# Optimization experiments

Measured on AMD Instinct MI355X. Metric: run time of the kernel, lower is better.

## Reference

```python
import jax, jax.numpy as jnp
import numpy as np


def conv1d(x, w, b, pad):
    # x: [B,C,T], w: [O,I,K]
    y = jax.lax.conv_general_dilated(x, w, (1,), [(pad, pad)],
                                     dimension_numbers=('NCH', 'OIH', 'NCH'))
    return y + b[None, :, None]


def setup_inputs() -> dict:
    key = jax.random.key(0)
    ks = jax.random.split(key, 16)
    s = 0.05
    return {
        'x':    jax.random.normal(ks[0], (1024, 512), dtype=jnp.float32),
        'w1':   jax.random.normal(ks[1], (5, 1, 3), dtype=jnp.float32) * s,
        'b1':   jnp.zeros((5,), jnp.float32),
        'w2':   jax.random.normal(ks[2], (10, 5, 5), dtype=jnp.float32) * s,
        'b2':   jnp.zeros((10,), jnp.float32),
        'w3':   jax.random.normal(ks[3], (10, 10, 7), dtype=jnp.float32) * s,
        'b3':   jnp.zeros((10,), jnp.float32),
        'code': jax.random.uniform(ks[4], (10, 32), dtype=jnp.float32),
        'd1w':  jax.random.normal(ks[5], (10, 10, 5), dtype=jnp.float32) * s,
        'd1b':  jnp.zeros((10,), jnp.float32),
        'd2w':  jax.random.normal(ks[6], (10, 10, 5), dtype=jnp.float32) * s,
        'd2b':  jnp.zeros((10,), jnp.float32),
        'fcw':  jax.random.normal(ks[7], (512, 5120), dtype=jnp.float32) * 0.01,
        'fcb':  jnp.zeros((512,), jnp.float32),
    }


def reference(x, w1, b1, w2, b2, w3, b3, code, d1w, d1b, d2w, d2b, fcw, fcb):
    B = x.shape[0]
    h = x[:, None, :]                                   # [B,1,512]
    h = jax.nn.relu(conv1d(h, w1, b1, 1))               # [B,5,512]
    h = jax.nn.relu(conv1d(h, w2, b2, 2))               # [B,10,512]
    h = jnp.tanh(conv1d(h, w3, b3, 3))                  # [B,10,512]
    # squared distance: sum_c (h[b,c,t] - code[c,k])^2 -> [B,512,32]
    x2 = jnp.sum(h * h, axis=1)                         # [B,512]
    cross = jnp.einsum('bct,ck->btk', h, code)          # [B,512,32]
    c2 = jnp.sum(code * code, axis=0)                   # [32]
    dist = x2[:, :, None] - 2.0 * cross + c2[None, None, :]
    prob = jax.nn.softmax(-dist, axis=-1)               # [B,512,32]
    q = jnp.einsum('btk,ck->btc', prob, code)           # [B,512,10]
    h = q.transpose(0, 2, 1)                            # [B,10,512]
    h = jax.nn.relu(conv1d(h, d1w, d1b, 2))
    h = jax.nn.relu(conv1d(h, d2w, d2b, 2))
    flat = h.reshape(B, -1)                             # [B,5120]
    return jnp.tanh(flat @ fcw.T + fcb)                 # [B,512]
```

## Files before the change

kernel.cpp:

```cpp
#include <hip/hip_runtime.h>
#include <hip/hip_bf16.h>

#define TT 512
#define RS 16
#define RH 8
#define NROW 528
#define K_FC 5120

typedef _Float16 h8 __attribute__((ext_vector_type(8)));
typedef float f32x16 __attribute__((ext_vector_type(16)));
typedef __attribute__((address_space(1))) const void GAS;
typedef __attribute__((address_space(3))) void LAS;

__device__ __forceinline__ float fast_tanh(float v) {
    float e = __expf(2.0f * v);
    return 1.0f - 2.0f / (e + 1.0f);
}
__device__ __forceinline__ unsigned pk(float a, float b) {
    return __builtin_bit_cast(unsigned, __builtin_amdgcn_cvt_pkrtz(a, b));
}

__global__ __launch_bounds__(256) void prep_wtab_kernel(
    const float* __restrict__ w2, const float* __restrict__ w3,
    const float* __restrict__ d1w, const float* __restrict__ d2w,
    const float* __restrict__ code, uint4* __restrict__ wtab,
    unsigned* __restrict__ c2tab)
{
    const int i = blockIdx.x * 256 + threadIdx.x;
    if (i < 1600) {
        const int lane = i & 63;
        const int o = lane & 31;
        const int hi = lane >> 5;
        h8 v = {};
        if (i < 320) {
            const int j = i >> 6;
            #pragma unroll
            for (int e = 0; e < 8; ++e) {
                int k = hi * 8 + e;
                if (o < 10 && k < 5) v[e] = (_Float16)w2[(o * 5 + k) * 5 + j];
            }
        } else if (i < 768) {
            const int j = (i - 320) >> 6;
            #pragma unroll
            for (int e = 0; e < 8; ++e) {
                int k = hi * 8 + e;
                if (o < 10 && k < 10) v[e] = (_Float16)w3[(o * 10 + k) * 7 + j];
            }
        } else if (i < 1088) {
            const int j = (i - 768) >> 6;
            #pragma unroll
            for (int e = 0; e < 8; ++e) {
                int k = hi * 8 + e;
                if (o < 10 && k < 10) v[e] = (_Float16)d1w[(o * 10 + k) * 5 + j];
            }
        } else if (i < 1408) {
            const int j = (i - 1088) >> 6;
            #pragma unroll
            for (int e = 0; e < 8; ++e) {
                int k = hi * 8 + e;
                if (o < 10 && k < 10) v[e] = (_Float16)d2w[(o * 10 + k) * 5 + j];
            }
        } else if (i < 1472) {
            #pragma unroll
            for (int e = 0; e < 8; ++e) {
                int ch = hi * 8 + e;
                if (ch < 10) v[e] = (_Float16)(2.0f * code[ch * 32 + o]);
            }
        } else {
            const int ks = (i - 1472) >> 6;
            #pragma unroll
            for (int e = 0; e < 8; ++e) {
                int kc = ks * 16 + hi * 8 + e;
                if (o < 10) v[e] = (_Float16)code[o * 32 + kc];
            }
        }
        wtab[i] = __builtin_bit_cast(uint4, v);
    } else if (i < 1632) {
        int k = i - 1600;
        float s = 0.f;
        for (int c = 0; c < 10; ++c) { float cv = code[c * 32 + k]; s = fmaf(cv, cv, s); }
        c2tab[k] = __float_as_uint(4.0f - s);
    }
}

template<int J, int P, int ACT>
__device__ __forceinline__ void conv_stage(
    const _Float16* __restrict__ src, _Float16* __restrict__ dst,
    const uint4* __restrict__ wtab, int wbase, const float* __restrict__ bsrc)
{
    const int tid = threadIdx.x;
    const int lane = tid & 63;
    const int wv = tid >> 6;
    const int l31 = lane & 31;
    const int hi = lane >> 5;

    uint4 wf[J];
    #pragma unroll
    for (int j = 0; j < J; ++j) wf[j] = wtab[wbase + j * 64 + lane];
    float bias[6];
    #pragma unroll
    for (int r = 0; r < 6; ++r) {
        int m = (r & 3) + 8 * (r >> 2) + 4 * hi;
        bias[r] = (m < 10) ? bsrc[m] : 0.f;
    }

    #pragma unroll 2
    for (int tile = 0; tile < 4; ++tile) {
        const int tcol = wv * 128 + tile * 32 + l31;
        f32x16 acc = {};
        #pragma unroll
        for (int j = 0; j < J; ++j) {
            h8 bf = *(const h8*)(src + (tcol + RH - P + j) * RS + hi * 8);
            acc = __builtin_amdgcn_mfma_f32_32x32x16_f16(
                __builtin_bit_cast(h8, wf[j]), bf, acc, 0, 0, 0);
        }
        float v[6];
        #pragma unroll
        for (int r = 0; r < 6; ++r) {
            float t = acc[r] + bias[r];
            v[r] = (ACT == 0) ? fmaxf(t, 0.f) : fast_tanh(t);
        }
        unsigned* drow = (unsigned*)(dst + (tcol + RH) * RS);
        uint2 s1v; s1v.x = pk(v[0], v[1]); s1v.y = pk(v[2], v[3]);
        *(uint2*)(drow + hi * 2) = s1v;
        if (!hi) drow[4] = pk(v[4], v[5]);
    }
}

template<int J, int P>
__device__ __forceinline__ void conv_stage_flat(
    const _Float16* __restrict__ src, _Float16* __restrict__ flatrow,
    const uint4* __restrict__ wtab, int wbase, const float* __restrict__ bsrc)
{
    const int tid = threadIdx.x;
    const int lane = tid & 63;
    const int wv = tid >> 6;
    const int l31 = lane & 31;
    const int hi = lane >> 5;

    uint4 wf[J];
    #pragma unroll
    for (int j = 0; j < J; ++j) wf[j] = wtab[wbase + j * 64 + lane];
    float bias[6];
    #pragma unroll
    for (int r = 0; r < 6; ++r) {
        int m = (r & 3) + 8 * (r >> 2) + 4 * hi;
        bias[r] = (m < 10) ? bsrc[m] : 0.f;
    }

    #pragma unroll 2
    for (int tile = 0; tile < 4; ++tile) {
        const int tcol = wv * 128 + tile * 32 + l31;
        f32x16 acc = {};
        #pragma unroll
        for (int j = 0; j < J; ++j) {
            h8 bf = *(const h8*)(src + (tcol + RH - P + j) * RS + hi * 8);
            acc = __builtin_amdgcn_mfma_f32_32x32x16_f16(
                __builtin_bit_cast(h8, wf[j]), bf, acc, 0, 0, 0);
        }
        #pragma unroll
        for (int r = 0; r < 4; ++r)
            flatrow[(r + 4 * hi) * TT + tcol] = (_Float16)fmaxf(acc[r] + bias[r], 0.f);
        if (!hi) {
            flatrow[8 * TT + tcol] = (_Float16)fmaxf(acc[4] + bias[4], 0.f);
            flatrow[9 * TT + tcol] = (_Float16)fmaxf(acc[5] + bias[5], 0.f);
        }
    }
}

__device__ __forceinline__ void vq_stage(
    const _Float16* __restrict__ src, _Float16* __restrict__ dst,
    const uint4* __restrict__ wtab, const unsigned* __restrict__ c2tab)
{
    const int tid = threadIdx.x;
    const int lane = tid & 63;
    const int wv = tid >> 6;
    const int l31 = lane & 31;
    const int hi = lane >> 5;

    const h8 wcr = __builtin_bit_cast(h8, wtab[1408 + lane]);
    const h8 wq0 = __builtin_bit_cast(h8, wtab[1472 + lane]);
    const h8 wq1 = __builtin_bit_cast(h8, wtab[1536 + lane]);
    float c2s[16];
    #pragma unroll
    for (int r = 0; r < 16; ++r)
        c2s[r] = __uint_as_float(c2tab[(r & 3) + 8 * (r >> 2) + 4 * hi]);

    #pragma unroll 2
    for (int tile = 0; tile < 4; ++tile) {
        const int tcol = wv * 128 + tile * 32 + l31;
        h8 bf = *(const h8*)(src + (tcol + RH) * RS + hi * 8);
        f32x16 sacc = {};
        sacc = __builtin_amdgcn_mfma_f32_32x32x16_f16(wcr, bf, sacc, 0, 0, 0);

        float e[16], sum = 0.f;
        #pragma unroll
        for (int r = 0; r < 16; ++r) { e[r] = __expf(sacc[r] + c2s[r]); sum += e[r]; }
        float inv = 1.0f / (sum + __shfl_xor(sum, 32));

        unsigned epk[8], sopk[8];
        #pragma unroll
        for (int q = 0; q < 8; ++q) epk[q] = pk(e[2 * q], e[2 * q + 1]);
        #pragma unroll
        for (int q = 0; q < 8; ++q) sopk[q] = (unsigned)__shfl_xor((int)epk[q], 32);

        uint4 b0u, b1u;
        b0u.x = hi ? sopk[2] : epk[0]; b0u.y = hi ? sopk[3] : epk[1];
        b0u.z = hi ? epk[2] : sopk[0]; b0u.w = hi ? epk[3] : sopk[1];
        b1u.x = hi ? sopk[6] : epk[4]; b1u.y = hi ? sopk[7] : epk[5];
        b1u.z = hi ? epk[6] : sopk[4]; b1u.w = hi ? epk[7] : sopk[5];

        f32x16 qacc = {};
        qacc = __builtin_amdgcn_mfma_f32_32x32x16_f16(wq0, __builtin_bit_cast(h8, b0u), qacc, 0, 0, 0);
        qacc = __builtin_amdgcn_mfma_f32_32x32x16_f16(wq1, __builtin_bit_cast(h8, b1u), qacc, 0, 0, 0);

        float v[6];
        #pragma unroll
        for (int r = 0; r < 6; ++r) v[r] = qacc[r] * inv;
        unsigned* drow = (unsigned*)(dst + (tcol + RH) * RS);
        uint2 s1v; s1v.x = pk(v[0], v[1]); s1v.y = pk(v[2], v[3]);
        *(uint2*)(drow + hi * 2) = s1v;
        if (!hi) drow[4] = pk(v[4], v[5]);
    }
}

__global__ __launch_bounds__(256, 4) void enc_dec_kernel(
    const float* __restrict__ x,
    const float* __restrict__ w1, const float* __restrict__ b1,
    const float* __restrict__ b2, const float* __restrict__ b3,
    const float* __restrict__ d1b, const float* __restrict__ d2b,
    const uint4* __restrict__ wtab, const unsigned* __restrict__ c2tab,
    _Float16* __restrict__ flat,
    const float* __restrict__ fcw, _Float16* __restrict__ fcw_h, int nenc)
{
    __shared__ __align__(16) _Float16 bufA[NROW * RS];
    __shared__ __align__(16) _Float16 bufB[NROW * RS];

    const int tid = threadIdx.x;
    const int bid = blockIdx.x;

    if (bid >= nenc) {
        int i = (bid - nenc) * 256 + tid;
        float4 a = ((const float4*)fcw)[i * 2];
        float4 b4 = ((const float4*)fcw)[i * 2 + 1];
        h8 v;
        v[0] = (_Float16)a.x;  v[1] = (_Float16)a.y;
        v[2] = (_Float16)a.z;  v[3] = (_Float16)a.w;
        v[4] = (_Float16)b4.x; v[5] = (_Float16)b4.y;
        v[6] = (_Float16)b4.z; v[7] = (_Float16)b4.w;
        *(h8*)&fcw_h[(size_t)i * 8] = v;
        return;
    }

    if (tid < 32) {
        int r = tid >> 1, half = tid & 1;
        int rowz = (r < 8) ? r : 512 + r;
        uint4 z = {0, 0, 0, 0};
        *(uint4*)(bufA + rowz * RS + half * 8) = z;
    }
    {
        uint4 z = {0, 0, 0, 0};
        uint4* pb = (uint4*)bufB;
        for (int i = tid; i < NROW * RS / 8; i += 256) pb[i] = z;
    }

    {
        const float* xrow = x + (size_t)bid * TT;
        const int t0 = tid * 2;
        float xm  = (t0 > 0) ? xrow[t0 - 1] : 0.f;
        float x0v = xrow[t0];
        float x1v = xrow[t0 + 1];
        float xp  = (t0 < TT - 2) ? xrow[t0 + 2] : 0.f;
        h8 r0 = {}, r1 = {};
        #pragma unroll
        for (int o = 0; o < 5; ++o) {
            float k0 = w1[o * 3], k1 = w1[o * 3 + 1], k2 = w1[o * 3 + 2], bb = b1[o];
            float a0 = fmaf(k0, xm,  fmaf(k1, x0v, fmaf(k2, x1v, bb)));
            float a1 = fmaf(k0, x0v, fmaf(k1, x1v, fmaf(k2, xp,  bb)));
            r0[o] = (_Float16)fmaxf(a0, 0.f);
            r1[o] = (_Float16)fmaxf(a1, 0.f);
        }
        h8 zz = {};
        *(h8*)&bufA[(t0 + RH) * RS] = r0;
        *(h8*)&bufA[(t0 + RH) * RS + 8] = zz;
        *(h8*)&bufA[(t0 + 1 + RH) * RS] = r1;
        *(h8*)&bufA[(t0 + 1 + RH) * RS + 8] = zz;
    }
    __syncthreads();

    conv_stage<5, 2, 0>(bufA, bufB, wtab, 0, b2);
    __syncthreads();
    conv_stage<7, 3, 1>(bufB, bufA, wtab, 320, b3);
    __syncthreads();
    vq_stage(bufA, bufB, wtab, c2tab);
    __syncthreads();
    conv_stage<5, 2, 0>(bufB, bufA, wtab, 768, d1b);
    __syncthreads();
    conv_stage_flat<5, 2>(bufA, flat + (size_t)bid * (10 * TT),
                          wtab, 1088, d2b);
}

__global__ __launch_bounds__(256, 1) void fc_partial_kernel(
    const _Float16* __restrict__ A,
    const _Float16* __restrict__ W,
    float* __restrict__ partial)
{
    __shared__ __align__(16) unsigned char smem[49152];

    const int tid = threadIdx.x;
    const int lane = tid & 63;
    const int w = tid >> 6;
    const int l31 = lane & 31;
    const int hi = lane >> 5;

    const int bid = blockIdx.x;
    const int tile = (bid & 7) | ((bid >> 5) << 3);
    const int ks4  = (bid >> 3) & 3;
    const int m0 = (tile >> 3) * 128;
    const int n0 = (tile & 7) * 64;
    const int kbase = ks4 * 1280;

    const _Float16* Asrc = A + (size_t)m0 * K_FC + kbase;
    const _Float16* Wsrc = W + (size_t)n0 * K_FC + kbase;

    f32x16 acc0 = {}, acc1 = {};

    auto stage = [&](int buf, int s) {
        unsigned char* Ad = smem + buf * 24576;
        unsigned char* Bd = Ad + 16384;
        const int k0 = s * 64;
        #pragma unroll
        for (int p = 0; p < 4; ++p) {
            const int idx = p * 256 + tid;
            const int row = idx >> 3;
            const int c = idx & 7;
            const int csrc = c ^ (row & 7);
            __builtin_amdgcn_global_load_lds(
                (GAS*)(Asrc + (size_t)row * K_FC + k0 + csrc * 8),
                (LAS*)(Ad + idx * 16), 16, 0, 0);
        }
        #pragma unroll
        for (int p = 0; p < 2; ++p) {
            const int idx = p * 256 + tid;
            const int row = idx >> 3;
            const int c = idx & 7;
            const int csrc = c ^ (row & 7);
            __builtin_amdgcn_global_load_lds(
                (GAS*)(Wsrc + (size_t)row * K_FC + k0 + csrc * 8),
                (LAS*)(Bd + idx * 16), 16, 0, 0);
        }
    };

    stage(0, 0);
    __syncthreads();

    for (int s = 0; s < 20; ++s) {
        const int cur = s & 1;
        if (s + 1 < 20) stage(cur ^ 1, s + 1);

        const unsigned char* Ab = smem + cur * 24576;
        const unsigned char* Bb = Ab + 16384;
        const int ar = w * 32 + l31;
        #pragma unroll
        for (int ks = 0; ks < 4; ++ks) {
            const int kc = ks * 2 + hi;
            h8 af  = *(const h8*)(Ab + ar * 128 + ((kc ^ (ar & 7)) << 4));
            h8 bf0 = *(const h8*)(Bb + l31 * 128 + ((kc ^ (l31 & 7)) << 4));
            h8 bf1 = *(const h8*)(Bb + (l31 + 32) * 128 + ((kc ^ ((l31 + 32) & 7)) << 4));
            acc0 = __builtin_amdgcn_mfma_f32_32x32x16_f16(af, bf0, acc0, 0, 0, 0);
            acc1 = __builtin_amdgcn_mfma_f32_32x32x16_f16(af, bf1, acc1, 0, 0, 0);
        }
        __syncthreads();
    }

    float* base = partial + (size_t)ks4 * (1024 * 512);
    #pragma unroll
    for (int r = 0; r < 16; ++r) {
        const int m = m0 + w * 32 + (r & 3) + 8 * (r >> 2) + 4 * hi;
        base[(size_t)m * 512 + n0 + l31]      = acc0[r];
        base[(size_t)m * 512 + n0 + 32 + l31] = acc1[r];
    }
}

__global__ __launch_bounds__(256) void fc_reduce_kernel(
    const float* __restrict__ partial, const float* __restrict__ bias,
    float* __restrict__ out)
{
    const int i = (blockIdx.x * 256 + threadIdx.x) * 2;
    float2 p0 = *(const float2*)&partial[i];
    float2 p1 = *(const float2*)&partial[524288 + i];
    float2 p2 = *(const float2*)&partial[1048576 + i];
    float2 p3 = *(const float2*)&partial[1572864 + i];
    const int n = i & 511;
    float s0 = p0.x + p1.x + p2.x + p3.x + bias[n];
    float s1 = p0.y + p1.y + p2.y + p3.y + bias[n + 1];
    float2 o;
    o.x = fast_tanh(s0);
    o.y = fast_tanh(s1);
    *(float2*)&out[i] = o;
}

extern "C" void kernel_launch(void* const* d_in, const int* in_sizes, int n_in,
                              void* d_out, int out_size, void* d_ws, size_t ws_size,
                              hipStream_t stream) {
    const float* x    = (const float*)d_in[0];
    const float* w1   = (const float*)d_in[1];
    const float* b1   = (const float*)d_in[2];
    const float* w2   = (const float*)d_in[3];
    const float* b2   = (const float*)d_in[4];
    const float* w3   = (const float*)d_in[5];
    const float* b3   = (const float*)d_in[6];
    const float* code = (const float*)d_in[7];
    const float* d1w  = (const float*)d_in[8];
    const float* d1b  = (const float*)d_in[9];
    const float* d2w  = (const float*)d_in[10];
    const float* d2b  = (const float*)d_in[11];
    const float* fcw  = (const float*)d_in[12];
    const float* fcb  = (const float*)d_in[13];
    float* out = (float*)d_out;

    _Float16* flat_h  = (_Float16*)d_ws;
    _Float16* fcw_h   = (_Float16*)((char*)d_ws + 10485760);
    float*    partial = (float*)((char*)d_ws + 16777216);
    uint4*    wtab    = (uint4*)((char*)d_ws + 25165824);
    unsigned* c2tab   = (unsigned*)((char*)d_ws + 25165824 + 25600);

    const int Bsz = in_sizes[0] / TT;

    prep_wtab_kernel<<<7, 256, 0, stream>>>(w2, w3, d1w, d2w, code, wtab, c2tab);
    enc_dec_kernel<<<Bsz + 1280, 256, 0, stream>>>(x, w1, b1, b2, b3, d1b, d2b,
                                                   wtab, c2tab, flat_h,
                                                   fcw, fcw_h, Bsz);
    fc_partial_kernel<<<256, 256, 0, stream>>>(flat_h, fcw_h, partial);
    fc_reduce_kernel<<<1024, 256, 0, stream>>>(partial, fcb, out);
}
```

Measured before the change: 47.69 us.

## Fuse split-K reduction into FC GEMM via per-tile atomic counter; split K eight ways

The FC GEMM now splits K eight ways instead of four, launching 512 blocks with two blocks per CU allowed. Each block writes its partial tile to a contiguous per-tile region, then bumps a per-tile atomic counter. The last-arriving block sums the eight partials, adds bias and applies tanh, so the separate reduce kernel launch goes away. The cost is twice the partial-buffer traffic and a serialized tail reduction done by a single block per tile. The counter is zeroed in the prep kernel.

```diff
diff --git a/kernel.cpp b/kernel.cpp
--- a/kernel.cpp
+++ b/kernel.cpp
@@ -24,7 +24,7 @@
     const float* __restrict__ w2, const float* __restrict__ w3,
     const float* __restrict__ d1w, const float* __restrict__ d2w,
     const float* __restrict__ code, uint4* __restrict__ wtab,
-    unsigned* __restrict__ c2tab)
+    unsigned* __restrict__ c2tab, unsigned* __restrict__ tilecnt)
 {
     const int i = blockIdx.x * 256 + threadIdx.x;
     if (i < 1600) {
@@ -80,6 +80,8 @@
         float s = 0.f;
         for (int c = 0; c < 10; ++c) { float cv = code[c * 32 + k]; s = fmaf(cv, cv, s); }
         c2tab[k] = __float_as_uint(4.0f - s);
+    } else if (i < 1696) {
+        tilecnt[i - 1632] = 0u;
     }
 }
 
@@ -300,10 +302,13 @@
                           wtab, 1088, d2b);
 }
 
-__global__ __launch_bounds__(256, 1) void fc_partial_kernel(
+__global__ __launch_bounds__(256, 2) void fc_partial_kernel(
     const _Float16* __restrict__ A,
     const _Float16* __restrict__ W,
-    float* __restrict__ partial)
+    const float* __restrict__ bias,
+    float* __restrict__ partial,
+    unsigned* __restrict__ tilecnt,
+    float* __restrict__ out)
 {
     __shared__ __align__(16) unsigned char smem[49152];
 
@@ -314,11 +319,13 @@
     const int hi = lane >> 5;
 
     const int bid = blockIdx.x;
-    const int tile = (bid & 7) | ((bid >> 5) << 3);
-    const int ks4  = (bid >> 3) & 3;
-    const int m0 = (tile >> 3) * 128;
-    const int n0 = (tile & 7) * 64;
-    const int kbase = ks4 * 1280;
+    const int nt  = bid & 7;
+    const int ks8 = (bid >> 3) & 7;
+    const int mt  = bid >> 6;
+    const int tile = mt * 8 + nt;
+    const int m0 = mt * 128;
+    const int n0 = nt * 64;
+    const int kbase = ks8 * 640;
 
     const _Float16* Asrc = A + (size_t)m0 * K_FC + kbase;
     const _Float16* Wsrc = W + (size_t)n0 * K_FC + kbase;
@@ -354,9 +361,9 @@
     stage(0, 0);
     __syncthreads();
 
-    for (int s = 0; s < 20; ++s) {
+    for (int s = 0; s < 10; ++s) {
         const int cur = s & 1;
-        if (s + 1 < 20) stage(cur ^ 1, s + 1);
+        if (s + 1 < 10) stage(cur ^ 1, s + 1);
 
         const unsigned char* Ab = smem + cur * 24576;
         const unsigned char* Bb = Ab + 16384;
@@ -373,31 +380,39 @@
         __syncthreads();
     }
 
-    float* base = partial + (size_t)ks4 * (1024 * 512);
+    float* base = partial + ((size_t)tile * 8 + ks8) * (128 * 64);
     #pragma unroll
     for (int r = 0; r < 16; ++r) {
-        const int m = m0 + w * 32 + (r & 3) + 8 * (r >> 2) + 4 * hi;
-        base[(size_t)m * 512 + n0 + l31]      = acc0[r];
-        base[(size_t)m * 512 + n0 + 32 + l31] = acc1[r];
-    }
-}
-
-__global__ __launch_bounds__(256) void fc_reduce_kernel(
-    const float* __restrict__ partial, const float* __restrict__ bias,
-    float* __restrict__ out)
-{
-    const int i = (blockIdx.x * 256 + threadIdx.x) * 2;
-    float2 p0 = *(const float2*)&partial[i];
-    float2 p1 = *(const float2*)&partial[524288 + i];
-    float2 p2 = *(const float2*)&partial[1048576 + i];
-    float2 p3 = *(const float2*)&partial[1572864 + i];
-    const int n = i & 511;
-    float s0 = p0.x + p1.x + p2.x + p3.x + bias[n];
-    float s1 = p0.y + p1.y + p2.y + p3.y + bias[n + 1];
-    float2 o;
-    o.x = fast_tanh(s0);
-    o.y = fast_tanh(s1);
-    *(float2*)&out[i] = o;
+        const int mloc = w * 32 + (r & 3) + 8 * (r >> 2) + 4 * hi;
+        base[mloc * 64 + l31]      = acc0[r];
+        base[mloc * 64 + 32 + l31] = acc1[r];
+    }
+
+    __threadfence();
+    __shared__ unsigned donecnt;
+    if (tid == 0) donecnt = atomicAdd(&tilecnt[tile], 1u);
+    __syncthreads();
+    if (donecnt != 7u) return;
+    __threadfence();
+
+    const float* tb = partial + (size_t)tile * (8 * 128 * 64);
+    for (int i = tid * 4; i < 128 * 64; i += 1024) {
+        float4 s = *(const float4*)&tb[i];
+        #pragma unroll
+        for (int ksr = 1; ksr < 8; ++ksr) {
+            float4 p = *(const float4*)&tb[ksr * 8192 + i];
+            s.x += p.x; s.y += p.y; s.z += p.z; s.w += p.w;
+        }
+        const int mloc = i >> 6;
+        const int nloc = i & 63;
+        float4 bv = *(const float4*)&bias[n0 + nloc];
+        float4 o;
+        o.x = fast_tanh(s.x + bv.x);
+        o.y = fast_tanh(s.y + bv.y);
+        o.z = fast_tanh(s.z + bv.z);
+        o.w = fast_tanh(s.w + bv.w);
+        *(float4*)&out[(size_t)(m0 + mloc) * 512 + n0 + nloc] = o;
+    }
 }
 
 extern "C" void kernel_launch(void* const* d_in, const int* in_sizes, int n_in,
@@ -422,15 +437,17 @@
     _Float16* flat_h  = (_Float16*)d_ws;
     _Float16* fcw_h   = (_Float16*)((char*)d_ws + 10485760);
     float*    partial = (float*)((char*)d_ws + 16777216);
-    uint4*    wtab    = (uint4*)((char*)d_ws + 25165824);
-    unsigned* c2tab   = (unsigned*)((char*)d_ws + 25165824 + 25600);
+    uint4*    wtab    = (uint4*)((char*)d_ws + 33554432);
+    unsigned* c2tab   = (unsigned*)((char*)d_ws + 33554432 + 25600);
+    unsigned* tilecnt = (unsigned*)((char*)d_ws + 33554432 + 25728);
 
     const int Bsz = in_sizes[0] / TT;
 
-    prep_wtab_kernel<<<7, 256, 0, stream>>>(w2, w3, d1w, d2w, code, wtab, c2tab);
+    prep_wtab_kernel<<<7, 256, 0, stream>>>(w2, w3, d1w, d2w, code, wtab,
+                                            c2tab, tilecnt);
     enc_dec_kernel<<<Bsz + 1280, 256, 0, stream>>>(x, w1, b1, b2, b3, d1b, d2b,
                                                    wtab, c2tab, flat_h,
                                                    fcw, fcw_h, Bsz);
-    fc_partial_kernel<<<256, 256, 0, stream>>>(flat_h, fcw_h, partial);
-    fc_reduce_kernel<<<1024, 256, 0, stream>>>(partial, fcb, out);
-}
+    fc_partial_kernel<<<512, 256, 0, stream>>>(flat_h, fcw_h, fcb,
+                                               partial, tilecnt, out);
+}
```

After: 113.9 us. 2.39x slower.
